# Kernel optimization log

Hardware: AMD Instinct MI355X
Metric: run time of the kernel (lower is better)

## Reference

```python
import jax, jax.numpy as jnp
import numpy as np

EPS = 1e-5  # BatchNorm eps


def _conv_bn_tanh(h, w, b, g, be, m, v):
    # 3x3 conv, stride 1, SAME padding (pad = k//2), NCHW / OIHW
    y = jax.lax.conv_general_dilated(
        h, w, window_strides=(1, 1), padding='SAME',
        dimension_numbers=('NCHW', 'OIHW', 'NCHW'))
    y = y + b[None, :, None, None]
    # BatchNorm inference: gamma * (y - mean) / sqrt(var + eps) + beta
    scale = g * jax.lax.rsqrt(v + EPS)
    y = y * scale[None, :, None, None] + (be - m * scale)[None, :, None, None]
    return jnp.tanh(y)


def _unfold3x3(x):
    # torch F.unfold(k=3, pad=1, stride=1) -> (N, C, 9, H, W), kernel positions row-major
    N, C, H, W = x.shape
    xp = jnp.pad(x, ((0, 0), (0, 0), (1, 1), (1, 1)))
    patches = [xp[:, :, i:i + H, j:j + W] for i in range(3) for j in range(3)]
    return jnp.stack(patches, axis=2)  # (N, C, 9, H, W)


def setup_inputs() -> dict:
    key = jax.random.key(0)
    ks = jax.random.split(key, 24)
    N, C, H, W = 8, 64, 128, 128
    INTER, FEAT, NB, KK = 64, 6, 6, 9
    d = {}
    d['x'] = jax.random.normal(ks[0], (N, C, H, W), jnp.float32)
    d['w0'] = jax.random.normal(ks[1], (INTER, C, 3, 3), jnp.float32) * 0.05
    d['b0'] = jax.random.normal(ks[2], (INTER,), jnp.float32) * 0.05
    d['g0'] = jax.random.uniform(ks[3], (INTER,), jnp.float32)
    d['be0'] = jax.random.normal(ks[4], (INTER,), jnp.float32) * 0.05
    d['m0'] = jax.random.normal(ks[5], (INTER,), jnp.float32) * 0.05
    d['v0'] = jax.random.uniform(ks[6], (INTER,), jnp.float32)
    d['wm'] = jax.random.normal(ks[7], (5, INTER, INTER, 3, 3), jnp.float32) * 0.05
    d['bm'] = jax.random.normal(ks[8], (5, INTER), jnp.float32) * 0.05
    d['gm'] = jax.random.uniform(ks[9], (5, INTER), jnp.float32)
    d['bem'] = jax.random.normal(ks[10], (5, INTER), jnp.float32) * 0.05
    d['mm'] = jax.random.normal(ks[11], (5, INTER), jnp.float32) * 0.05
    d['vm'] = jax.random.uniform(ks[12], (5, INTER), jnp.float32)
    OC = FEAT * NB  # 36
    d['wl'] = jax.random.normal(ks[13], (OC, INTER, 3, 3), jnp.float32) * 0.05
    d['bl'] = jax.random.normal(ks[14], (OC,), jnp.float32) * 0.05
    d['gl'] = jax.random.uniform(ks[15], (OC,), jnp.float32)
    d['bel'] = jax.random.normal(ks[16], (OC,), jnp.float32) * 0.05
    d['ml'] = jax.random.normal(ks[17], (OC,), jnp.float32) * 0.05
    d['vl'] = jax.random.uniform(ks[18], (OC,), jnp.float32)
    d['bases'] = jax.random.normal(ks[19], (NB, KK), jnp.float32)  # FB bases buffer (6, 9)
    return d


def reference(x, w0, b0, g0, be0, m0, v0, wm, bm, gm, bem, mm, vm,
              wl, bl, gl, bel, ml, vl, bases):
    N, C, H, W = x.shape
    FEAT, NB = 6, 6
    # bases_net: conv-bn-tanh x7 (eval mode, dropout no-ops)
    h = _conv_bn_tanh(x, w0, b0, g0, be0, m0, v0)
    for i in range(5):
        h = _conv_bn_tanh(h, wm[i], bm[i], gm[i], bem[i], mm[i], vm[i])
    h = _conv_bn_tanh(h, wl, bl, gl, bel, ml, vl)  # (N, 36, H, W)
    bfeat = h.reshape(N, FEAT, NB, H, W)
    # per-pixel basis coefficients: (N, M, 9, H, W)
    bcoef = jnp.einsum('bmkhw,kl->bmlhw', bfeat, bases)
    patches = _unfold3x3(x)  # (N, C, 9, H, W)
    # dynamic conv: combine per-pixel coeffs with unfolded input
    out = jnp.einsum('bmlhw,bclhw->bcmhw', bcoef, patches)  # (N, C, M, H, W)
    return out.reshape(N, C * NB, H, W)
```

## Files before the change

### kernel.cpp

```cpp
#include <hip/hip_runtime.h>
#include <hip/hip_bf16.h>

typedef short bf16x4 __attribute__((ext_vector_type(4)));
typedef short bf16x8 __attribute__((ext_vector_type(8)));
typedef float f32x4  __attribute__((ext_vector_type(4)));

__device__ inline unsigned short f2us(float f) {
    __hip_bfloat16 h = __float2bfloat16(f);
    return *(unsigned short*)&h;
}
__device__ inline float us2f(unsigned short u) {
    union { unsigned int i; float f; } c; c.i = ((unsigned int)u) << 16; return c.f;
}
__device__ inline float tanh_fast(float x) {
    float xs = fminf(fmaxf(x, -20.f), 20.f);
    float t = __expf(2.f * xs);
    return 1.f - 2.f / (t + 1.f);
}

__device__ inline void gload_lds16(const void* g, void* l) {
    __builtin_amdgcn_global_load_lds(
        (const __attribute__((address_space(1))) void*)g,
        (__attribute__((address_space(3))) void*)l,
        16, 0, 0);
}

__global__ __launch_bounds__(256)
void prep_all(const float* __restrict__ x, unsigned short* __restrict__ xcl,
              const float* __restrict__ w0, const float* __restrict__ wm,
              const float* __restrict__ wl, unsigned short* __restrict__ Wf,
              const float* b0, const float* g0, const float* be0,
              const float* m0, const float* v0,
              const float* bm, const float* gm, const float* bem,
              const float* mm, const float* vm,
              const float* bl, const float* gl, const float* bel,
              const float* ml, const float* vl,
              float* __restrict__ Af, float* __restrict__ Bf,
              unsigned int* __restrict__ zp)
{
    const int bid = blockIdx.x;
    const int t = threadIdx.x;
    if (bid < 1024) {
        __shared__ unsigned short t2[128 * 68];
        int n = bid >> 7, h = bid & 127;
        const float* xp = x + (size_t)n * 64 * 16384 + h * 128;
        for (int i = t; i < 8192; i += 256) {
            int ci = i >> 7, w = i & 127;
            t2[w * 68 + ci] = f2us(xp[(size_t)ci * 16384 + w]);
        }
        __syncthreads();
        unsigned short* op = xcl + ((size_t)(n * 16384 + h * 128)) * 64;
        for (int i = t; i < 1024; i += 256) {
            int w = i >> 3, c8 = i & 7;
            union { bf16x4 v[2]; uint4 q; } u;
            u.v[0] = *(bf16x4*)&t2[w * 68 + c8 * 8];
            u.v[1] = *(bf16x4*)&t2[w * 68 + c8 * 8 + 4];
            *(uint4*)(op + w * 64 + c8 * 8) = u.q;
        }
    } else if (bid < 2032) {
        int idx = (bid - 1024) * 256 + t;
        int l = idx / 36864, r = idx - l * 36864;
        int tp = r >> 12, r2 = r & 4095;
        int hh = r2 >> 11, nb = (r2 >> 9) & 3, ln = (r2 >> 3) & 63, j = r2 & 7;
        int ci = hh * 32 + (ln >> 4) * 8 + j;
        int co = (ln & 15) * 4 + nb;
        float val = 0.f;
        if (l < 6) {
            const float* src = (l == 0) ? w0 : (wm + (size_t)(l - 1) * 36864);
            val = src[(co * 64 + ci) * 9 + tp];
        } else if (co < 36) {
            val = wl[(co * 64 + ci) * 9 + tp];
        }
        Wf[idx] = f2us(val);
    } else {
        int idx = (bid - 2032) * 256 + t;
        if (bid == 2033 && t >= 192) zp[t - 192] = 0u;
        if (idx < 448) {
            int l = idx >> 6, c = idx & 63;
            float b, g, be, m, v;
            bool zero = false;
            if (l == 0) {
                b = b0[c]; g = g0[c]; be = be0[c]; m = m0[c]; v = v0[c];
            } else if (l < 6) {
                int o = (l - 1) * 64 + c;
                b = bm[o]; g = gm[o]; be = bem[o]; m = mm[o]; v = vm[o];
            } else if (c < 36) {
                b = bl[c]; g = gl[c]; be = bel[c]; m = ml[c]; v = vl[c];
            } else zero = true;
            if (zero) { Af[idx] = 0.f; Bf[idx] = 0.f; }
            else {
                float s = g / sqrtf(v + 1e-5f);
                Af[idx] = s;
                Bf[idx] = (b - m) * s + be;
            }
        }
    }
}

#define LDS_W_OFF 78336
__global__ __launch_bounds__(512, 2)
void conv_mfma(const unsigned short* __restrict__ src,
               const unsigned short* __restrict__ Wf,
               const float* __restrict__ A, const float* __restrict__ B,
               unsigned short* __restrict__ dst,
               const unsigned short* __restrict__ zp)
{
    __shared__ __align__(16) unsigned char smem[152064];
    const int n = blockIdx.z;
    const int h0 = blockIdx.y * 16, w0 = blockIdx.x * 32;
    const int t = threadIdx.x;
    const int ln = t & 63, wv = t >> 6;
    const int xln = ln & 15, qd = ln >> 4;
    const size_t ibase = (size_t)n * 16384 * 64;

    const unsigned short* srcn = src + ibase;
    for (int i = wv; i < 77; i += 8) {
        int g = i * 64 + ln;
        int p = g >> 3, jj = g & 7;
        int ty = (p * 1928) >> 16;
        int tx = p - ty * 34;
        int gy = h0 + ty - 1, gx = w0 + tx - 1;
        int js = jj ^ (p & 7);
        const unsigned short* gsrc =
            (((unsigned)gy < 128u) & ((unsigned)gx < 128u))
                ? srcn + (ptrdiff_t)(gy * 128 + gx) * 64 + js * 8
                : zp;
        if (g < 4896) gload_lds16(gsrc, smem + (size_t)i * 1024);
    }
    for (int i = wv; i < 72; i += 8) {
        const unsigned short* gsrc = Wf + ((size_t)(i * 64 + ln)) * 8;
        gload_lds16(gsrc, smem + LDS_W_OFF + (size_t)i * 1024);
    }
    __syncthreads();

    f32x4 acc[2][2][4];
#pragma unroll
    for (int rh = 0; rh < 2; ++rh)
#pragma unroll
        for (int hf = 0; hf < 2; ++hf)
#pragma unroll
            for (int nb = 0; nb < 4; ++nb)
                acc[rh][hf][nb] = (f32x4){0.f, 0.f, 0.f, 0.f};

    const int rbase = wv * 2;
#pragma unroll
    for (int tp = 0; tp < 9; ++tp) {
        const int ky = tp / 3, kx = tp % 3;
        bf16x8 b[2][4];
#pragma unroll
        for (int hh = 0; hh < 2; ++hh)
#pragma unroll
            for (int nb = 0; nb < 4; ++nb)
                b[hh][nb] = *(const bf16x8*)(smem + LDS_W_OFF +
                    (((((tp * 2 + hh) * 4 + nb) * 64) + ln) << 4));
#pragma unroll
        for (int rh = 0; rh < 2; ++rh) {
#pragma unroll
            for (int hf = 0; hf < 2; ++hf) {
                const int p = (rbase + rh + ky) * 34 + hf * 16 + xln + kx;
                const int pb = p * 128, sw = (p & 7) << 4;
#pragma unroll
                for (int hh = 0; hh < 2; ++hh) {
                    bf16x8 a = *(const bf16x8*)(smem + pb +
                                                (((qd + 4 * hh) << 4) ^ sw));
#pragma unroll
                    for (int nb = 0; nb < 4; ++nb)
                        acc[rh][hf][nb] = __builtin_amdgcn_mfma_f32_16x16x32_bf16(
                            a, b[hh][nb], acc[rh][hf][nb], 0, 0, 0);
                }
            }
        }
    }

    const float4 A4 = *(const float4*)&A[xln * 4];
    const float4 B4 = *(const float4*)&B[xln * 4];
#pragma unroll
    for (int rh = 0; rh < 2; ++rh) {
        const int gy = h0 + rbase + rh;
        unsigned short* dp = dst + ibase + (size_t)(gy * 128) * 64 + xln * 4;
#pragma unroll
        for (int hf = 0; hf < 2; ++hf) {
#pragma unroll
            for (int r = 0; r < 4; ++r) {
                const int gx = w0 + hf * 16 + qd * 4 + r;
                ushort4 o;
                o.x = f2us(tanh_fast(fmaf(acc[rh][hf][0][r], A4.x, B4.x)));
                o.y = f2us(tanh_fast(fmaf(acc[rh][hf][1][r], A4.y, B4.y)));
                o.z = f2us(tanh_fast(fmaf(acc[rh][hf][2][r], A4.z, B4.z)));
                o.w = f2us(tanh_fast(fmaf(acc[rh][hf][3][r], A4.w, B4.w)));
                *(ushort4*)(dp + (size_t)gx * 64) = o;
            }
        }
    }
}

__global__ __launch_bounds__(256)
void dyn_conv(const float* __restrict__ x, const unsigned short* __restrict__ h7,
              const float* __restrict__ bases, float* __restrict__ out)
{
    __shared__ float tile[32 * 10 * 34];
    const int n = blockIdx.z;
    const int h0 = blockIdx.y * 8, w0 = blockIdx.x * 32;
    const float* xp = x + (size_t)n * 64 * 16384;
    const int t = threadIdx.x;
    const int tw = t & 31, th = t >> 5;
    const int h = h0 + th, w = w0 + tw;

    float bs[54];
#pragma unroll
    for (int i = 0; i < 54; ++i) bs[i] = bases[i];

    union { uint4 q[5]; unsigned short s[40]; } hv;
    const unsigned short* hp = h7 + (size_t)(n * 16384 + h * 128 + w) * 64;
#pragma unroll
    for (int i = 0; i < 5; ++i) hv.q[i] = ((const uint4*)hp)[i];

    float coef[54];
#pragma unroll
    for (int i = 0; i < 54; ++i) coef[i] = 0.f;
#pragma unroll
    for (int m = 0; m < 6; ++m)
#pragma unroll
        for (int k = 0; k < 6; ++k) {
            float f = us2f(hv.s[m * 6 + k]);
#pragma unroll
            for (int l = 0; l < 9; ++l)
                coef[m * 9 + l] = fmaf(f, bs[k * 9 + l], coef[m * 9 + l]);
        }

    float* op = out + (size_t)n * 384 * 16384 + h * 128 + w;

    for (int half = 0; half < 2; ++half) {
        if (half) __syncthreads();
        for (int idx = t; idx < 32 * 340; idx += 256) {
            int ci = idx / 340, r = idx % 340, y = r / 34, xw = r % 34;
            int gy = h0 + y - 1, gx = w0 + xw - 1;
            float v = 0.f;
            if ((unsigned)gy < 128u && (unsigned)gx < 128u)
                v = xp[(size_t)(half * 32 + ci) * 16384 + gy * 128 + gx];
            tile[idx] = v;
        }
        __syncthreads();

#pragma unroll 1
        for (int c = 0; c < 32; ++c) {
            float xv[9];
#pragma unroll
            for (int ky = 0; ky < 3; ++ky)
#pragma unroll
                for (int kx = 0; kx < 3; ++kx)
                    xv[ky * 3 + kx] = tile[c * 340 + (th + ky) * 34 + (tw + kx)];
            int cg = half * 32 + c;
#pragma unroll
            for (int m = 0; m < 6; ++m) {
                float s = 0.f;
#pragma unroll
                for (int l = 0; l < 9; ++l) s = fmaf(coef[m * 9 + l], xv[l], s);
                op[(size_t)(cg * 6 + m) * 16384] = s;
            }
        }
    }
}

extern "C" void kernel_launch(void* const* d_in, const int* in_sizes, int n_in,
                              void* d_out, int out_size, void* d_ws, size_t ws_size,
                              hipStream_t stream)
{
    const float* x   = (const float*)d_in[0];
    const float* w0  = (const float*)d_in[1];
    const float* b0  = (const float*)d_in[2];
    const float* g0  = (const float*)d_in[3];
    const float* be0 = (const float*)d_in[4];
    const float* m0  = (const float*)d_in[5];
    const float* v0  = (const float*)d_in[6];
    const float* wm  = (const float*)d_in[7];
    const float* bm  = (const float*)d_in[8];
    const float* gm  = (const float*)d_in[9];
    const float* bem = (const float*)d_in[10];
    const float* mm  = (const float*)d_in[11];
    const float* vm  = (const float*)d_in[12];
    const float* wl  = (const float*)d_in[13];
    const float* bl  = (const float*)d_in[14];
    const float* gl  = (const float*)d_in[15];
    const float* bel = (const float*)d_in[16];
    const float* ml  = (const float*)d_in[17];
    const float* vl  = (const float*)d_in[18];
    const float* bas = (const float*)d_in[19];

    unsigned short* Wfb = (unsigned short*)d_ws;
    float* Af  = (float*)((char*)d_ws + 524288);
    float* Bf  = Af + 448;
    unsigned int* zp = (unsigned int*)((char*)d_ws + (1 << 20));
    unsigned short* xcl  = (unsigned short*)((char*)d_ws + (size_t)(2  << 20));
    unsigned short* bufA = (unsigned short*)((char*)d_ws + (size_t)(2  << 20) + 16777216);
    unsigned short* bufB = (unsigned short*)((char*)d_ws + (size_t)(2  << 20) + 2 * 16777216);

    prep_all<<<2034, 256, 0, stream>>>(x, xcl, w0, wm, wl, Wfb,
                                       b0, g0, be0, m0, v0,
                                       bm, gm, bem, mm, vm,
                                       bl, gl, bel, ml, vl, Af, Bf, zp);

    dim3 cg(4, 8, 8);
    const unsigned short* zps = (const unsigned short*)zp;
    conv_mfma<<<cg, 512, 0, stream>>>(xcl,  Wfb + 0 * 36864, Af + 0,   Bf + 0,   bufA, zps);
    conv_mfma<<<cg, 512, 0, stream>>>(bufA, Wfb + 1 * 36864, Af + 64,  Bf + 64,  bufB, zps);
    conv_mfma<<<cg, 512, 0, stream>>>(bufB, Wfb + 2 * 36864, Af + 128, Bf + 128, bufA, zps);
    conv_mfma<<<cg, 512, 0, stream>>>(bufA, Wfb + 3 * 36864, Af + 192, Bf + 192, bufB, zps);
    conv_mfma<<<cg, 512, 0, stream>>>(bufB, Wfb + 4 * 36864, Af + 256, Bf + 256, bufA, zps);
    conv_mfma<<<cg, 512, 0, stream>>>(bufA, Wfb + 5 * 36864, Af + 320, Bf + 320, bufB, zps);
    conv_mfma<<<cg, 512, 0, stream>>>(bufB, Wfb + 6 * 36864, Af + 384, Bf + 384, bufA, zps);

    dim3 dg(4, 16, 8);
    dyn_conv<<<dg, 256, 0, stream>>>(x, bufA, bas, (float*)d_out);
}
```

Measured before the change: 403.7 us.

## Fuse all conv layers and dynamic conv into one persistent cooperative kernel

Replaces the seven per-layer conv launches and the dynamic-conv launch with a single cooperative kernel. Each block keeps its spatial tile's activations in LDS across layers, publishes only its border pixels to global memory, and waits on per-neighbour flags before pulling in halo rows and columns. Next-layer weights are prefetched into registers while the MFMA loop runs, and the final layer's output goes straight to LDS for the dynamic conv. This removes the full activation round-trips through global memory and the kernel launch gaps, at the cost of spin-wait synchronisation, a flag scheme that relies on values from prior calls not colliding, and a requirement that all 256 blocks be co-resident.

```diff
diff --git a/kernel.cpp b/kernel.cpp
--- a/kernel.cpp
+++ b/kernel.cpp
@@ -97,166 +97,281 @@
     }
 }
 
+struct Mega2Args {
+    const float *x, *bas, *Af, *Bf;
+    const unsigned short *xcl, *Wfb, *zp;
+    unsigned short *s0, *s1;
+    unsigned long long *flags;
+    float *out;
+};
+
 #define LDS_W_OFF 78336
-__global__ __launch_bounds__(512, 2)
-void conv_mfma(const unsigned short* __restrict__ src,
-               const unsigned short* __restrict__ Wf,
-               const float* __restrict__ A, const float* __restrict__ B,
-               unsigned short* __restrict__ dst,
-               const unsigned short* __restrict__ zp)
+#define FLAGV(v) ((0xAB5EED00ULL << 32) | (unsigned long long)(v))
+
+#define MFMA_BLOCK(ACC)                                                        \
+    _Pragma("unroll")                                                          \
+    for (int tp = 0; tp < 9; ++tp) {                                           \
+        const int ky = tp / 3, kx = tp % 3;                                    \
+        bf16x8 bfr[2][4];                                                      \
+        _Pragma("unroll")                                                      \
+        for (int hh = 0; hh < 2; ++hh)                                         \
+            _Pragma("unroll")                                                  \
+            for (int nb = 0; nb < 4; ++nb)                                     \
+                bfr[hh][nb] = *(const bf16x8*)(smem + LDS_W_OFF +              \
+                    (((((tp * 2 + hh) * 4 + nb) * 64) + ln) << 4));            \
+        _Pragma("unroll")                                                      \
+        for (int rh = 0; rh < 2; ++rh) {                                       \
+            _Pragma("unroll")                                                  \
+            for (int hf = 0; hf < 2; ++hf) {                                   \
+                const int p = (rbase + rh + ky) * 34 + hf * 16 + xln + kx;     \
+                const int pb = p * 128, sw = (p & 7) << 4;                     \
+                _Pragma("unroll")                                              \
+                for (int hh = 0; hh < 2; ++hh) {                               \
+                    bf16x8 afr = *(const bf16x8*)(smem + pb +                  \
+                                        (((qd + 4 * hh) << 4) ^ sw));          \
+                    _Pragma("unroll")                                          \
+                    for (int nb = 0; nb < 4; ++nb)                             \
+                        ACC[rh][hf][nb] =                                      \
+                            __builtin_amdgcn_mfma_f32_16x16x32_bf16(           \
+                                afr, bfr[hh][nb], ACC[rh][hf][nb], 0, 0, 0);   \
+                }                                                              \
+            }                                                                  \
+        }                                                                      \
+    }
+
+__global__ __launch_bounds__(512, 2) void mega2(Mega2Args g)
 {
     __shared__ __align__(16) unsigned char smem[152064];
-    const int n = blockIdx.z;
-    const int h0 = blockIdx.y * 16, w0 = blockIdx.x * 32;
+    const int bid = blockIdx.x;
+    const int bx = bid & 3, by = (bid >> 2) & 7, cn = bid >> 5;
+    const int h0 = by * 16, w0c = bx * 32;
     const int t = threadIdx.x;
     const int ln = t & 63, wv = t >> 6;
     const int xln = ln & 15, qd = ln >> 4;
-    const size_t ibase = (size_t)n * 16384 * 64;
-
-    const unsigned short* srcn = src + ibase;
-    for (int i = wv; i < 77; i += 8) {
-        int g = i * 64 + ln;
-        int p = g >> 3, jj = g & 7;
-        int ty = (p * 1928) >> 16;
-        int tx = p - ty * 34;
-        int gy = h0 + ty - 1, gx = w0 + tx - 1;
-        int js = jj ^ (p & 7);
-        const unsigned short* gsrc =
-            (((unsigned)gy < 128u) & ((unsigned)gx < 128u))
-                ? srcn + (ptrdiff_t)(gy * 128 + gx) * 64 + js * 8
-                : zp;
-        if (g < 4896) gload_lds16(gsrc, smem + (size_t)i * 1024);
+    const int rbase = wv * 2;
+    const size_t ibase = (size_t)cn * 16384 * 64;
+
+    {
+        const unsigned short* srcn = g.xcl + ibase;
+        for (int i = wv; i < 77; i += 8) {
+            int gg = i * 64 + ln;
+            int p = gg >> 3, jj = gg & 7;
+            int ty = (p * 1928) >> 16;
+            int tx = p - ty * 34;
+            int gy = h0 + ty - 1, gx = w0c + tx - 1;
+            int js = jj ^ (p & 7);
+            const unsigned short* gsrc =
+                (((unsigned)gy < 128u) & ((unsigned)gx < 128u))
+                    ? srcn + (ptrdiff_t)(gy * 128 + gx) * 64 + js * 8
+                    : g.zp;
+            if (gg < 4896) gload_lds16(gsrc, smem + (size_t)i * 1024);
+        }
+        for (int i = wv; i < 72; i += 8)
+            gload_lds16(g.Wfb + ((size_t)(i * 64 + ln)) * 8,
+                        smem + LDS_W_OFF + (size_t)i * 1024);
+        __syncthreads();
     }
-    for (int i = wv; i < 72; i += 8) {
-        const unsigned short* gsrc = Wf + ((size_t)(i * 64 + ln)) * 8;
-        gload_lds16(gsrc, smem + LDS_W_OFF + (size_t)i * 1024);
+
+#pragma unroll 1
+    for (int l = 0; l < 6; ++l) {
+        uint4 wpre[9];
+        {
+            const uint4* wnext = (const uint4*)(g.Wfb + (size_t)(l + 1) * 36864);
+#pragma unroll
+            for (int k = 0; k < 9; ++k) wpre[k] = wnext[t + 512 * k];
+        }
+
+        f32x4 acc[2][2][4];
+#pragma unroll
+        for (int rh = 0; rh < 2; ++rh)
+#pragma unroll
+            for (int hf = 0; hf < 2; ++hf)
+#pragma unroll
+                for (int nb = 0; nb < 4; ++nb)
+                    acc[rh][hf][nb] = (f32x4){0.f, 0.f, 0.f, 0.f};
+
+        MFMA_BLOCK(acc);
+
+        __syncthreads();
+
+        unsigned short* stripb = (l & 1) ? g.s1 : g.s0;
+        const float4 A4 = *(const float4*)&g.Af[l * 64 + xln * 4];
+        const float4 B4 = *(const float4*)&g.Bf[l * 64 + xln * 4];
+        const int cchunk = xln >> 1, coff = (xln & 1) * 8;
+#pragma unroll
+        for (int rh = 0; rh < 2; ++rh) {
+            const int oy = rbase + rh;
+#pragma unroll
+            for (int hf = 0; hf < 2; ++hf) {
+#pragma unroll
+                for (int r = 0; r < 4; ++r) {
+                    const int ox = hf * 16 + qd * 4 + r;
+                    union { ushort4 s; unsigned long long u; } o;
+                    o.s.x = f2us(tanh_fast(fmaf(acc[rh][hf][0][r], A4.x, B4.x)));
+                    o.s.y = f2us(tanh_fast(fmaf(acc[rh][hf][1][r], A4.y, B4.y)));
+                    o.s.z = f2us(tanh_fast(fmaf(acc[rh][hf][2][r], A4.z, B4.z)));
+                    o.s.w = f2us(tanh_fast(fmaf(acc[rh][hf][3][r], A4.w, B4.w)));
+                    const int p = (oy + 1) * 34 + (ox + 1);
+                    *(unsigned long long*)(smem + p * 128 +
+                        (((cchunk ^ (p & 7)) << 4) | coff)) = o.u;
+                    if (oy == 0 || oy == 15 || ox == 0 || ox == 31) {
+                        unsigned long long* sp = (unsigned long long*)(stripb +
+                            ibase + (size_t)((h0 + oy) * 128 + (w0c + ox)) * 64 +
+                            xln * 4);
+                        __hip_atomic_store(sp, o.u, __ATOMIC_RELAXED,
+                                           __HIP_MEMORY_SCOPE_AGENT);
+                    }
+                }
+            }
+        }
+        {
+            uint4* wdst = (uint4*)(smem + LDS_W_OFF);
+#pragma unroll
+            for (int k = 0; k < 9; ++k) wdst[t + 512 * k] = wpre[k];
+        }
+        asm volatile("s_waitcnt vmcnt(0)" ::: "memory");
+        __syncthreads();
+
+        if (t == 0)
+            __hip_atomic_store(&g.flags[bid], FLAGV(l + 1),
+                               __ATOMIC_RELAXED, __HIP_MEMORY_SCOPE_AGENT);
+        if (t < 8) {
+            int tt = t + (t >= 4);
+            int dx = tt % 3 - 1, dy = tt / 3 - 1;
+            int nbx = bx + dx, nby = by + dy;
+            if (((unsigned)nbx < 4u) & ((unsigned)nby < 8u)) {
+                const unsigned long long* fp =
+                    g.flags + (cn * 32 + nby * 4 + nbx);
+                const unsigned long long tgt = FLAGV(l + 1);
+                while (__hip_atomic_load(fp, __ATOMIC_RELAXED,
+                                         __HIP_MEMORY_SCOPE_AGENT) != tgt)
+                    __builtin_amdgcn_s_sleep(2);
+            }
+        }
+        __syncthreads();
+
+        for (int idx = t; idx < 1600; idx += 512) {
+            int p5 = idx >> 4, j2 = idx & 15;
+            int ty, tx;
+            if (p5 < 34)      { ty = 0;  tx = p5; }
+            else if (p5 < 68) { ty = 17; tx = p5 - 34; }
+            else { int k = p5 - 68; ty = 1 + (k >> 1); tx = (k & 1) ? 33 : 0; }
+            int gy = h0 + ty - 1, gx = w0c + tx - 1;
+            unsigned long long v = 0ull;
+            if (((unsigned)gy < 128u) & ((unsigned)gx < 128u)) {
+                const unsigned long long* sp = (const unsigned long long*)(stripb +
+                    ibase + (size_t)(gy * 128 + gx) * 64) + j2;
+                v = __hip_atomic_load(sp, __ATOMIC_RELAXED,
+                                      __HIP_MEMORY_SCOPE_AGENT);
+            }
+            int p = ty * 34 + tx;
+            *(unsigned long long*)(smem + p * 128 +
+                ((((j2 >> 1) ^ (p & 7)) << 4) | ((j2 & 1) * 8))) = v;
+        }
+        __syncthreads();
     }
-    __syncthreads();
-
-    f32x4 acc[2][2][4];
-#pragma unroll
-    for (int rh = 0; rh < 2; ++rh)
-#pragma unroll
-        for (int hf = 0; hf < 2; ++hf)
-#pragma unroll
-            for (int nb = 0; nb < 4; ++nb)
-                acc[rh][hf][nb] = (f32x4){0.f, 0.f, 0.f, 0.f};
-
-    const int rbase = wv * 2;
-#pragma unroll
-    for (int tp = 0; tp < 9; ++tp) {
-        const int ky = tp / 3, kx = tp % 3;
-        bf16x8 b[2][4];
-#pragma unroll
-        for (int hh = 0; hh < 2; ++hh)
-#pragma unroll
-            for (int nb = 0; nb < 4; ++nb)
-                b[hh][nb] = *(const bf16x8*)(smem + LDS_W_OFF +
-                    (((((tp * 2 + hh) * 4 + nb) * 64) + ln) << 4));
+
+    {
+        f32x4 acc[2][2][4];
+#pragma unroll
+        for (int rh = 0; rh < 2; ++rh)
+#pragma unroll
+            for (int hf = 0; hf < 2; ++hf)
+#pragma unroll
+                for (int nb = 0; nb < 4; ++nb)
+                    acc[rh][hf][nb] = (f32x4){0.f, 0.f, 0.f, 0.f};
+        MFMA_BLOCK(acc);
+        __syncthreads();
+
+        unsigned short* h7 = (unsigned short*)(smem + LDS_W_OFF);
+        const float4 A4 = *(const float4*)&g.Af[6 * 64 + xln * 4];
+        const float4 B4 = *(const float4*)&g.Bf[6 * 64 + xln * 4];
+        const int cchunk = xln >> 1, coff = (xln & 1) * 8;
 #pragma unroll
         for (int rh = 0; rh < 2; ++rh) {
 #pragma unroll
             for (int hf = 0; hf < 2; ++hf) {
-                const int p = (rbase + rh + ky) * 34 + hf * 16 + xln + kx;
-                const int pb = p * 128, sw = (p & 7) << 4;
-#pragma unroll
-                for (int hh = 0; hh < 2; ++hh) {
-                    bf16x8 a = *(const bf16x8*)(smem + pb +
-                                                (((qd + 4 * hh) << 4) ^ sw));
-#pragma unroll
-                    for (int nb = 0; nb < 4; ++nb)
-                        acc[rh][hf][nb] = __builtin_amdgcn_mfma_f32_16x16x32_bf16(
-                            a, b[hh][nb], acc[rh][hf][nb], 0, 0, 0);
+#pragma unroll
+                for (int r = 0; r < 4; ++r) {
+                    const int pl = (rbase + rh) * 32 + hf * 16 + qd * 4 + r;
+                    ushort4 o;
+                    o.x = f2us(tanh_fast(fmaf(acc[rh][hf][0][r], A4.x, B4.x)));
+                    o.y = f2us(tanh_fast(fmaf(acc[rh][hf][1][r], A4.y, B4.y)));
+                    o.z = f2us(tanh_fast(fmaf(acc[rh][hf][2][r], A4.z, B4.z)));
+                    o.w = f2us(tanh_fast(fmaf(acc[rh][hf][3][r], A4.w, B4.w)));
+                    *(ushort4*)((unsigned char*)h7 + pl * 128 +
+                                (((cchunk ^ (pl & 7)) << 4) | coff)) = o;
                 }
             }
         }
-    }
-
-    const float4 A4 = *(const float4*)&A[xln * 4];
-    const float4 B4 = *(const float4*)&B[xln * 4];
-#pragma unroll
-    for (int rh = 0; rh < 2; ++rh) {
-        const int gy = h0 + rbase + rh;
-        unsigned short* dp = dst + ibase + (size_t)(gy * 128) * 64 + xln * 4;
-#pragma unroll
-        for (int hf = 0; hf < 2; ++hf) {
-#pragma unroll
-            for (int r = 0; r < 4; ++r) {
-                const int gx = w0 + hf * 16 + qd * 4 + r;
-                ushort4 o;
-                o.x = f2us(tanh_fast(fmaf(acc[rh][hf][0][r], A4.x, B4.x)));
-                o.y = f2us(tanh_fast(fmaf(acc[rh][hf][1][r], A4.y, B4.y)));
-                o.z = f2us(tanh_fast(fmaf(acc[rh][hf][2][r], A4.z, B4.z)));
-                o.w = f2us(tanh_fast(fmaf(acc[rh][hf][3][r], A4.w, B4.w)));
-                *(ushort4*)(dp + (size_t)gx * 64) = o;
-            }
-        }
-    }
-}
-
-__global__ __launch_bounds__(256)
-void dyn_conv(const float* __restrict__ x, const unsigned short* __restrict__ h7,
-              const float* __restrict__ bases, float* __restrict__ out)
-{
-    __shared__ float tile[32 * 10 * 34];
-    const int n = blockIdx.z;
-    const int h0 = blockIdx.y * 8, w0 = blockIdx.x * 32;
-    const float* xp = x + (size_t)n * 64 * 16384;
-    const int t = threadIdx.x;
-    const int tw = t & 31, th = t >> 5;
-    const int h = h0 + th, w = w0 + tw;
-
-    float bs[54];
-#pragma unroll
-    for (int i = 0; i < 54; ++i) bs[i] = bases[i];
-
-    union { uint4 q[5]; unsigned short s[40]; } hv;
-    const unsigned short* hp = h7 + (size_t)(n * 16384 + h * 128 + w) * 64;
-#pragma unroll
-    for (int i = 0; i < 5; ++i) hv.q[i] = ((const uint4*)hp)[i];
-
-    float coef[54];
-#pragma unroll
-    for (int i = 0; i < 54; ++i) coef[i] = 0.f;
-#pragma unroll
-    for (int m = 0; m < 6; ++m)
-#pragma unroll
-        for (int k = 0; k < 6; ++k) {
-            float f = us2f(hv.s[m * 6 + k]);
-#pragma unroll
-            for (int l = 0; l < 9; ++l)
-                coef[m * 9 + l] = fmaf(f, bs[k * 9 + l], coef[m * 9 + l]);
-        }
-
-    float* op = out + (size_t)n * 384 * 16384 + h * 128 + w;
-
-    for (int half = 0; half < 2; ++half) {
-        if (half) __syncthreads();
-        for (int idx = t; idx < 32 * 340; idx += 256) {
-            int ci = idx / 340, r = idx % 340, y = r / 34, xw = r % 34;
-            int gy = h0 + y - 1, gx = w0 + xw - 1;
-            float v = 0.f;
-            if ((unsigned)gy < 128u && (unsigned)gx < 128u)
-                v = xp[(size_t)(half * 32 + ci) * 16384 + gy * 128 + gx];
-            tile[idx] = v;
-        }
-        __syncthreads();
+        __syncthreads();
+
+        const int pxx = t & 31, py = t >> 5;
+        const int h = h0 + py, w = w0c + pxx;
+
+        float bs[54];
+#pragma unroll
+        for (int i = 0; i < 54; ++i) bs[i] = g.bas[i];
+
+        union { uint4 q[5]; unsigned short s[40]; } hv;
+        {
+            const int pl = py * 32 + pxx;
+            const unsigned char* hb = smem + LDS_W_OFF + pl * 128;
+#pragma unroll
+            for (int j = 0; j < 5; ++j)
+                hv.q[j] = *(const uint4*)(hb + ((j ^ (pl & 7)) << 4));
+        }
+
+        float coef[54];
+#pragma unroll
+        for (int i = 0; i < 54; ++i) coef[i] = 0.f;
+#pragma unroll
+        for (int m = 0; m < 6; ++m)
+#pragma unroll
+            for (int k = 0; k < 6; ++k) {
+                float f = us2f(hv.s[m * 6 + k]);
+#pragma unroll
+                for (int lq = 0; lq < 9; ++lq)
+                    coef[m * 9 + lq] = fmaf(f, bs[k * 9 + lq], coef[m * 9 + lq]);
+            }
+
+        const float* xp = g.x + (size_t)cn * 64 * 16384;
+        float* op = g.out + (size_t)cn * 384 * 16384 + h * 128 + w;
+        float* tile = (float*)smem;
+
+        for (int half = 0; half < 2; ++half) {
+            __syncthreads();
+            for (int idx = t; idx < 19584; idx += 512) {
+                int y = ((idx >> 6) * 3856) >> 16;
+                int rem = idx - y * 1088;
+                int ci = (rem * 1928) >> 16;
+                int xw = rem - ci * 34;
+                int gy = h0 + y - 1, gx = w0c + xw - 1;
+                float v = 0.f;
+                if ((unsigned)gy < 128u && (unsigned)gx < 128u)
+                    v = xp[(size_t)(half * 32 + ci) * 16384 + gy * 128 + gx];
+                tile[ci * 612 + y * 34 + xw] = v;
+            }
+            __syncthreads();
 
 #pragma unroll 1
-        for (int c = 0; c < 32; ++c) {
-            float xv[9];
-#pragma unroll
-            for (int ky = 0; ky < 3; ++ky)
-#pragma unroll
-                for (int kx = 0; kx < 3; ++kx)
-                    xv[ky * 3 + kx] = tile[c * 340 + (th + ky) * 34 + (tw + kx)];
-            int cg = half * 32 + c;
-#pragma unroll
-            for (int m = 0; m < 6; ++m) {
-                float s = 0.f;
-#pragma unroll
-                for (int l = 0; l < 9; ++l) s = fmaf(coef[m * 9 + l], xv[l], s);
-                op[(size_t)(cg * 6 + m) * 16384] = s;
+            for (int c = 0; c < 32; ++c) {
+                float xv[9];
+#pragma unroll
+                for (int ky = 0; ky < 3; ++ky)
+#pragma unroll
+                    for (int kx = 0; kx < 3; ++kx)
+                        xv[ky * 3 + kx] =
+                            tile[c * 612 + (py + ky) * 34 + (pxx + kx)];
+                int cgc = half * 32 + c;
+#pragma unroll
+                for (int m = 0; m < 6; ++m) {
+                    float s = 0.f;
+#pragma unroll
+                    for (int lq = 0; lq < 9; ++lq)
+                        s = fmaf(coef[m * 9 + lq], xv[lq], s);
+                    op[(size_t)(cgc * 6 + m) * 16384] = s;
+                }
             }
         }
     }
@@ -291,25 +406,24 @@
     float* Af  = (float*)((char*)d_ws + 524288);
     float* Bf  = Af + 448;
     unsigned int* zp = (unsigned int*)((char*)d_ws + (1 << 20));
-    unsigned short* xcl  = (unsigned short*)((char*)d_ws + (size_t)(2  << 20));
-    unsigned short* bufA = (unsigned short*)((char*)d_ws + (size_t)(2  << 20) + 16777216);
-    unsigned short* bufB = (unsigned short*)((char*)d_ws + (size_t)(2  << 20) + 2 * 16777216);
+    unsigned long long* flags =
+        (unsigned long long*)((char*)d_ws + (1 << 20) + 4096);
+    unsigned short* xcl  = (unsigned short*)((char*)d_ws + (size_t)(2 << 20));
+    unsigned short* bufA = (unsigned short*)((char*)d_ws + (size_t)(2 << 20) + 16777216);
+    unsigned short* bufB = (unsigned short*)((char*)d_ws + (size_t)(2 << 20) + 2 * 16777216);
 
     prep_all<<<2034, 256, 0, stream>>>(x, xcl, w0, wm, wl, Wfb,
                                        b0, g0, be0, m0, v0,
                                        bm, gm, bem, mm, vm,
                                        bl, gl, bel, ml, vl, Af, Bf, zp);
 
-    dim3 cg(4, 8, 8);
-    const unsigned short* zps = (const unsigned short*)zp;
-    conv_mfma<<<cg, 512, 0, stream>>>(xcl,  Wfb + 0 * 36864, Af + 0,   Bf + 0,   bufA, zps);
-    conv_mfma<<<cg, 512, 0, stream>>>(bufA, Wfb + 1 * 36864, Af + 64,  Bf + 64,  bufB, zps);
-    conv_mfma<<<cg, 512, 0, stream>>>(bufB, Wfb + 2 * 36864, Af + 128, Bf + 128, bufA, zps);
-    conv_mfma<<<cg, 512, 0, stream>>>(bufA, Wfb + 3 * 36864, Af + 192, Bf + 192, bufB, zps);
-    conv_mfma<<<cg, 512, 0, stream>>>(bufB, Wfb + 4 * 36864, Af + 256, Bf + 256, bufA, zps);
-    conv_mfma<<<cg, 512, 0, stream>>>(bufA, Wfb + 5 * 36864, Af + 320, Bf + 320, bufB, zps);
-    conv_mfma<<<cg, 512, 0, stream>>>(bufB, Wfb + 6 * 36864, Af + 384, Bf + 384, bufA, zps);
-
-    dim3 dg(4, 16, 8);
-    dyn_conv<<<dg, 256, 0, stream>>>(x, bufA, bas, (float*)d_out);
-}
+    Mega2Args a;
+    a.x = x; a.bas = bas; a.Af = Af; a.Bf = Bf;
+    a.xcl = xcl; a.Wfb = Wfb; a.zp = (const unsigned short*)zp;
+    a.s0 = bufA; a.s1 = bufB;
+    a.flags = flags;
+    a.out = (float*)d_out;
+
+    void* ka[] = {&a};
+    hipLaunchCooperativeKernel((const void*)mega2, dim3(256), dim3(512), ka, 0, stream);
+}
```

Measured after the change: 442.2 us. 9.5% more time.
